# Kernel optimization log

Measured on AMD Instinct MI355X. Metric: run time of the kernel, lower is better.

The kernel has to match this reference:

```python
import jax, jax.numpy as jnp
import numpy as np

HIDDEN = 256
HEADS = 4
HEAD_DIM = HIDDEN // HEADS
SCALE = HEAD_DIM ** -0.5
N1, N2 = 6000, 6000


def setup_inputs() -> dict:
    key = jax.random.key(0)
    ks = jax.random.split(key, 12)
    s = 1.0 / np.sqrt(HIDDEN)
    return {
        "kg1_emb": jax.random.normal(ks[0], (N1, HIDDEN), jnp.float32),
        "kg2_emb": jax.random.normal(ks[1], (N2, HIDDEN), jnp.float32),
        "alignment_matrix": jax.random.bernoulli(ks[2], 0.01, (N1, N2)).astype(jnp.float32),
        "Wq": jax.random.normal(ks[3], (HIDDEN, HIDDEN), jnp.float32) * s,
        "bq": jnp.zeros((HIDDEN,), jnp.float32),
        "Wk": jax.random.normal(ks[4], (HIDDEN, HIDDEN), jnp.float32) * s,
        "bk": jnp.zeros((HIDDEN,), jnp.float32),
        "Wv": jax.random.normal(ks[5], (HIDDEN, HIDDEN), jnp.float32) * s,
        "bv": jnp.zeros((HIDDEN,), jnp.float32),
        "Wo": jax.random.normal(ks[6], (HIDDEN, HIDDEN), jnp.float32) * s,
        "bo": jnp.zeros((HIDDEN,), jnp.float32),
    }


def _cross_attend(q_emb, kv_emb, align, Wq, bq, Wk, bk, Wv, bv):
    # q_emb: [Nq, H*D], kv_emb: [Nk, H*D], align: [Nq, Nk]
    Nq, Nk = q_emb.shape[0], kv_emb.shape[0]
    Q = (q_emb @ Wq.T + bq).reshape(Nq, HEADS, HEAD_DIM)
    K = (kv_emb @ Wk.T + bk).reshape(Nk, HEADS, HEAD_DIM)
    V = (kv_emb @ Wv.T + bv).reshape(Nk, HEADS, HEAD_DIM)
    # einsum('nih,mjh->nmij').mean(-1) == Q against head-mean of K (same math)
    Kbar = K.mean(axis=1)  # [Nk, D]
    scores = jnp.einsum('nid,md->nmi', Q, Kbar) * SCALE  # [Nq, Nk, HEADS]
    scores = scores * align[:, :, None]                  # multiplicative mask
    w = jax.nn.softmax(scores, axis=1)                   # over kv entities
    out = jnp.einsum('nmh,mhd->nhd', w, V)               # [Nq, HEADS, D]
    return out.reshape(Nq, HIDDEN)


def reference(kg1_emb, kg2_emb, alignment_matrix, Wq, bq, Wk, bk, Wv, bv, Wo, bo):
    kg1_from_kg2 = _cross_attend(kg1_emb, kg2_emb, alignment_matrix,
                                 Wq, bq, Wk, bk, Wv, bv)
    kg1_enhanced = kg1_emb + (kg1_from_kg2 @ Wo.T + bo)
    kg2_from_kg1 = _cross_attend(kg2_emb, kg1_emb, alignment_matrix.T,
                                 Wq, bq, Wk, bk, Wv, bv)
    kg2_enhanced = kg2_emb + (kg2_from_kg1 @ Wo.T + bo)
    return (kg1_enhanced, kg2_enhanced)
```

## Files before the change

### kernel.cpp

```cpp
#include <hip/hip_runtime.h>
#include <hip/hip_bf16.h>
#include <stdint.h>

typedef __bf16 bf16_t;
typedef __bf16 bf16x8 __attribute__((ext_vector_type(8)));
typedef __bf16 bf16x4 __attribute__((ext_vector_type(4)));
typedef float f32x4 __attribute__((ext_vector_type(4)));

#define NROW 6000
#define HID 256
#define NHEAD 4
#define HD 64
#define ATT_SCALE 0.125f
#define MTOT 12000
#define CAP 128
#define NCHUNK 4500000

__global__ __launch_bounds__(256)
void detect_kernel(const unsigned short* __restrict__ a, int* __restrict__ flag)
{
    int k = blockIdx.x * 256 + threadIdx.x;
    int found = (k < 102400 && a[2 * k] != 0) ? 1 : 0;
    if (__ballot(found)) {
        if ((threadIdx.x & 63) == 0) atomicOr(flag, 1);
    }
}

__global__ __launch_bounds__(256)
void canon_all_kernel(const void* __restrict__ e1, const void* __restrict__ e2,
                      const void* __restrict__ wq, const void* __restrict__ wk,
                      const void* __restrict__ wv, const void* __restrict__ wo,
                      const void* __restrict__ bq, const void* __restrict__ bk,
                      const void* __restrict__ bv, const void* __restrict__ bo,
                      bf16_t* __restrict__ cE, bf16_t* __restrict__ cWB,
                      const int* __restrict__ flag)
{
    __shared__ int fb;
    if (threadIdx.x == 0) fb = *flag;
    __syncthreads();
    int i = blockIdx.x * 256 + threadIdx.x;
    const int NE = NROW * HID;
    const int NW = 4 * HID * HID;
    auto conv = [&](const void* s, int k) -> bf16_t {
        return fb ? ((const bf16_t*)s)[k] : (bf16_t)(((const float*)s)[k]);
    };
    if (i < 2 * NE) {
        cE[i] = (i < NE) ? conv(e1, i) : conv(e2, i - NE);
        return;
    }
    i -= 2 * NE;
    if (i < NW) {
        int seg = i >> 16; int k = i & 65535;
        const void* s = (seg == 0) ? wq : (seg == 1) ? wk : (seg == 2) ? wv : wo;
        cWB[i] = conv(s, k);
        return;
    }
    i -= NW;
    if (i < 4 * HID) {
        int seg = i >> 8; int k = i & 255;
        const void* s = (seg == 0) ? bq : (seg == 1) ? bk : (seg == 2) ? bv : bo;
        cWB[NW + i] = conv(s, k);
    }
}

__global__ __launch_bounds__(256)
void proj_qkv_kernel(const bf16_t* __restrict__ e12,
                     const bf16_t* __restrict__ wq, const bf16_t* __restrict__ wk,
                     const bf16_t* __restrict__ wv,
                     const bf16_t* __restrict__ bq, const bf16_t* __restrict__ bk,
                     const bf16_t* __restrict__ bv,
                     float* __restrict__ Q, bf16_t* __restrict__ Kf, bf16_t* __restrict__ V)
{
    int m0   = blockIdx.x * 64;
    int n0   = blockIdx.y * 64;
    int wave = threadIdx.x >> 6;
    int lane = threadIdx.x & 63;
    int r16  = lane & 15;
    int quad = lane >> 4;

    int sel = n0 >> 8;
    int jb  = n0 & 255;
    const bf16_t* W; const bf16_t* bias;
    if (sel == 0)      { W = wq; bias = bq; }
    else if (sel == 1) { W = wk; bias = bk; }
    else               { W = wv; bias = bv; }

    int arow = m0 + wave * 16 + r16;
    int rr   = arow < MTOT ? arow : MTOT - 1;
    const bf16_t* asrc = e12 + (size_t)rr * HID;

    f32x4 acc0 = {0,0,0,0}, acc1 = {0,0,0,0}, acc2 = {0,0,0,0}, acc3 = {0,0,0,0};
#pragma unroll
    for (int kk = 0; kk < HID; kk += 32) {
        bf16x8 a = *(const bf16x8*)(asrc + kk + quad * 8);
        const bf16_t* b0 = W + (size_t)(jb + r16) * HID + kk + quad * 8;
        bf16x8 f0 = *(const bf16x8*)(b0);
        bf16x8 f1 = *(const bf16x8*)(b0 + 16 * HID);
        bf16x8 f2 = *(const bf16x8*)(b0 + 32 * HID);
        bf16x8 f3 = *(const bf16x8*)(b0 + 48 * HID);
        acc0 = __builtin_amdgcn_mfma_f32_16x16x32_bf16(a, f0, acc0, 0, 0, 0);
        acc1 = __builtin_amdgcn_mfma_f32_16x16x32_bf16(a, f1, acc1, 0, 0, 0);
        acc2 = __builtin_amdgcn_mfma_f32_16x16x32_bf16(a, f2, acc2, 0, 0, 0);
        acc3 = __builtin_amdgcn_mfma_f32_16x16x32_bf16(a, f3, acc3, 0, 0, 0);
    }
    f32x4 accs[4] = {acc0, acc1, acc2, acc3};
    int rbase = m0 + wave * 16 + quad * 4;
#pragma unroll
    for (int nt = 0; nt < 4; ++nt) {
        int j = jb + nt * 16 + r16;
        float bb = (float)bias[j];
#pragma unroll
        for (int rg = 0; rg < 4; ++rg) {
            int r = rbase + rg;
            if (r < MTOT) {
                float v = accs[nt][rg] + bb;
                if (sel == 0)      Q [(size_t)r * HID + j] = v;
                else if (sel == 1) Kf[(size_t)r * HID + j] = (bf16_t)v;
                else               V [(size_t)r * HID + j] = (bf16_t)v;
            }
        }
    }
}

__global__ __launch_bounds__(256)
void kbar_vsum_kernel(const bf16_t* __restrict__ Kf, const bf16_t* __restrict__ V,
                      bf16_t* __restrict__ Kbar, float* __restrict__ Vsum)
{
    int b = blockIdx.x;
    if (b < 3000) {
        int id = b * 256 + threadIdx.x;
        int m = id >> 6, d = id & 63;
        const bf16_t* kr = Kf + (size_t)m * HID + d;
        Kbar[id] = (bf16_t)(0.25f * ((float)kr[0] + (float)kr[64] +
                                     (float)kr[128] + (float)kr[192]));
    } else {
        int idx = b - 3000;
        int g = idx >> 5 ? 1 : (idx >= 24 ? 1 : 0);
        g = idx / 24;
        int seg = idx - g * 24;
        int j = threadIdx.x;
        const bf16_t* base = V + ((size_t)(g * NROW + seg * 250)) * HID + j;
        float s = 0.f;
        for (int m = 0; m < 250; ++m) s += (float)base[(size_t)m * HID];
        atomicAdd(Vsum + g * HID + j, s);
    }
}

__global__ __launch_bounds__(256)
void scan_nz_kernel(const void* __restrict__ av,
                    int* __restrict__ rcur,
                    int* __restrict__ csr,
                    const int* __restrict__ flag)
{
    __shared__ int fb;
    if (threadIdx.x == 0) fb = *flag;
    __syncthreads();
    int lane = threadIdx.x & 63;
    int ch   = blockIdx.x * 256 + threadIdx.x;
    bool oob = (ch >= NCHUNK);
    int che  = oob ? (NCHUNK - 1) : ch;

    unsigned int nzmask = 0;
    if (!oob) {
        if (fb) {
            uint4 u = *(const uint4*)((const unsigned short*)av + (size_t)che * 8);
            unsigned int w[4] = {u.x, u.y, u.z, u.w};
#pragma unroll
            for (int p = 0; p < 4; ++p) {
                if (w[p] & 0xFFFFu)  nzmask |= 1u << (2 * p);
                if (w[p] >> 16)      nzmask |= 1u << (2 * p + 1);
            }
        } else {
            const unsigned int* aw = (const unsigned int*)av + (size_t)che * 8;
            uint4 u0 = *(const uint4*)(aw);
            uint4 u1 = *(const uint4*)(aw + 4);
            unsigned int w[8] = {u0.x, u0.y, u0.z, u0.w, u1.x, u1.y, u1.z, u1.w};
#pragma unroll
            for (int p = 0; p < 8; ++p)
                if (w[p]) nzmask |= 1u << p;
        }
    }
    int n  = che / 750;
    int m0 = (che - n * 750) * 8;
    int c  = __popc(nzmask);

    int p = c;
#pragma unroll
    for (int off = 1; off < 64; off <<= 1) {
        int t = __shfl_up(p, off);
        if (lane >= off) p += t;
    }
    int excl  = p - c;
    int total = __shfl(p, 63);

    int nFirst = __shfl(n, 0);
    int nLast  = __shfl(n, 63);
    unsigned long long mb = __ballot(n == nLast);
    int s0  = __ffsll(mb) - 1;
    int pS0 = __shfl(excl, s0);

    int baseB = 0;
    if (lane == s0) {
        int totalB = total - pS0;
        if (totalB > 0) baseB = atomicAdd(rcur + nLast, totalB);
    }
    baseB = __shfl(baseB, s0);
    int baseA = 0;
    if (s0 > 0) {
        if (lane == 0 && pS0 > 0) baseA = atomicAdd(rcur + nFirst, pS0);
        baseA = __shfl(baseA, 0);
    }

    int myOff = (n == nLast) ? (baseB + excl - pS0) : (baseA + excl);
    if (c) {
        int* dst = csr + (size_t)n * CAP;
        int w = 0;
#pragma unroll
        for (int pb = 0; pb < 8; ++pb) {
            if (nzmask & (1u << pb)) {
                int idx = myOff + (w++);
                if (idx < CAP) dst[idx] = m0 + pb;
            }
        }
    }
}

__global__ __launch_bounds__(256)
void csc_kernel(const int* __restrict__ rcnt, const int* __restrict__ csr,
                int* __restrict__ ccur, int* __restrict__ csc)
{
    int tid = blockIdx.x * 256 + threadIdx.x;
    int n = tid >> 7, j = tid & (CAP - 1);
    if (n >= NROW) return;
    int cnt = rcnt[n]; if (cnt > CAP) cnt = CAP;
    if (j >= cnt) return;
    int m = csr[(size_t)n * CAP + j];
    int slot = atomicAdd(ccur + m, 1);
    if (slot < CAP) csc[(size_t)m * CAP + slot] = n;
}

__global__ __launch_bounds__(256)
void attn_kernel(const float* __restrict__ Q, const bf16_t* __restrict__ Kbar,
                 const bf16_t* __restrict__ V, const float* __restrict__ Vsum,
                 const int* __restrict__ rcnt, const int* __restrict__ ccnt,
                 const int* __restrict__ csr, const int* __restrict__ csc,
                 bf16_t* __restrict__ att)
{
    __shared__ float qs[HID];
    __shared__ int   ml[CAP];
    __shared__ float sc[CAP * 5];
    __shared__ float w0s[NHEAD];
    __shared__ __align__(16) bf16_t kbs[CAP * HD];

    int dir = blockIdx.y;
    int n   = blockIdx.x;
    int t   = threadIdx.x;
    int wave = t >> 6, lane = t & 63;

    size_t qrow = (size_t)(dir ? NROW + n : n);
    const bf16_t* kb_base = Kbar + (dir ? 0 : (size_t)NROW * HD);
    const bf16_t* v_base  = V    + (dir ? 0 : (size_t)NROW * HID);
    const float*  vs      = Vsum + (dir ? 0 : HID);
    const int*    lst     = (dir ? csc : csr) + (size_t)n * CAP;
    int cnt = (dir ? ccnt : rcnt)[n];
    if (cnt > CAP) cnt = CAP;

    qs[t] = Q[qrow * HID + t];
    for (int j = t; j < cnt; j += 256) ml[j] = lst[j];
    __syncthreads();

    for (int j = wave; j < cnt; j += 4) {
        int m = ml[j];
        bf16_t v = kb_base[(size_t)m * HD + lane];
        kbs[j * HD + ((((lane >> 3) + j) & 7) << 3) + (lane & 7)] = v;
    }
    __syncthreads();

    {
        int head = wave;
        const float* qh = qs + head * HD;
        for (int jb2 = 0; jb2 < cnt; jb2 += 64) {
            int j = jb2 + lane;
            if (j < cnt) {
                float dot = 0.f;
#pragma unroll
                for (int c = 0; c < 8; ++c) {
                    bf16x8 k8 = *(const bf16x8*)(kbs + j * HD + (((c + j) & 7) << 3));
#pragma unroll
                    for (int i = 0; i < 8; ++i)
                        dot += qh[c * 8 + i] * (float)k8[i];
                }
                sc[j * 5 + head] = dot * ATT_SCALE;
            }
        }
    }
    __syncthreads();

    {
        int head = wave;
        float M = 0.0f;
        for (int j = lane; j < cnt; j += 64) M = fmaxf(M, sc[j * 5 + head]);
        for (int off = 32; off; off >>= 1) M = fmaxf(M, __shfl_xor(M, off));
        float e0 = __expf(-M);
        float e[2]; int k = 0;
        float S = 0.f;
        for (int j = lane; j < cnt; j += 64, ++k) { e[k] = __expf(sc[j * 5 + head] - M); S += e[k]; }
        for (int off = 32; off; off >>= 1) S += __shfl_xor(S, off);
        float Z = S + (float)(NROW - cnt) * e0;
        float invZ = 1.0f / Z;
        k = 0;
        for (int j = lane; j < cnt; j += 64, ++k) sc[j * 5 + head] = (e[k] - e0) * invZ;
        if (lane == 0) w0s[head] = e0 * invZ;
    }
    __syncthreads();

    int h3 = lane >> 4;
    int dq = lane & 15;
    int colb = h3 * HD + dq * 4;
    float a0 = 0.f, a1 = 0.f, a2 = 0.f, a3 = 0.f;
    {
        int j = wave;
        for (; j + 4 < cnt; j += 8) {
            int   m0 = ml[j];            int   m1 = ml[j + 4];
            float c0 = sc[j * 5 + h3];   float c1 = sc[(j + 4) * 5 + h3];
            bf16x4 r0 = *(const bf16x4*)(v_base + (size_t)m0 * HID + colb);
            bf16x4 r1 = *(const bf16x4*)(v_base + (size_t)m1 * HID + colb);
            a0 += c0 * (float)r0[0] + c1 * (float)r1[0];
            a1 += c0 * (float)r0[1] + c1 * (float)r1[1];
            a2 += c0 * (float)r0[2] + c1 * (float)r1[2];
            a3 += c0 * (float)r0[3] + c1 * (float)r1[3];
        }
        if (j < cnt) {
            int   m0 = ml[j];
            float c0 = sc[j * 5 + h3];
            bf16x4 r0 = *(const bf16x4*)(v_base + (size_t)m0 * HID + colb);
            a0 += c0 * (float)r0[0];
            a1 += c0 * (float)r0[1];
            a2 += c0 * (float)r0[2];
            a3 += c0 * (float)r0[3];
        }
    }
    __syncthreads();
    float* red = (float*)kbs;
    red[wave * 256 + colb + 0] = a0;
    red[wave * 256 + colb + 1] = a1;
    red[wave * 256 + colb + 2] = a2;
    red[wave * 256 + colb + 3] = a3;
    __syncthreads();
    float tot = red[t] + red[256 + t] + red[512 + t] + red[768 + t]
              + w0s[t >> 6] * vs[t];
    att[qrow * HID + t] = (bf16_t)tot;
}

__global__ __launch_bounds__(256)
void proj_out_kernel(const bf16_t* __restrict__ att, const bf16_t* __restrict__ wo,
                     const bf16_t* __restrict__ bo,
                     const void* __restrict__ e1v, const void* __restrict__ e2v,
                     void* __restrict__ outv, const int* __restrict__ flag)
{
    __shared__ int fb;
    if (threadIdx.x == 0) fb = *flag;
    __syncthreads();

    int m0   = blockIdx.x * 64;
    int n0   = blockIdx.y * 64;
    int wave = threadIdx.x >> 6;
    int lane = threadIdx.x & 63;
    int r16  = lane & 15;
    int quad = lane >> 4;

    int arow = m0 + wave * 16 + r16;
    int rr   = arow < MTOT ? arow : MTOT - 1;
    const bf16_t* asrc = att + (size_t)rr * HID;

    f32x4 acc0 = {0,0,0,0}, acc1 = {0,0,0,0}, acc2 = {0,0,0,0}, acc3 = {0,0,0,0};
#pragma unroll
    for (int kk = 0; kk < HID; kk += 32) {
        bf16x8 a = *(const bf16x8*)(asrc + kk + quad * 8);
        const bf16_t* b0 = wo + (size_t)(n0 + r16) * HID + kk + quad * 8;
        bf16x8 f0 = *(const bf16x8*)(b0);
        bf16x8 f1 = *(const bf16x8*)(b0 + 16 * HID);
        bf16x8 f2 = *(const bf16x8*)(b0 + 32 * HID);
        bf16x8 f3 = *(const bf16x8*)(b0 + 48 * HID);
        acc0 = __builtin_amdgcn_mfma_f32_16x16x32_bf16(a, f0, acc0, 0, 0, 0);
        acc1 = __builtin_amdgcn_mfma_f32_16x16x32_bf16(a, f1, acc1, 0, 0, 0);
        acc2 = __builtin_amdgcn_mfma_f32_16x16x32_bf16(a, f2, acc2, 0, 0, 0);
        acc3 = __builtin_amdgcn_mfma_f32_16x16x32_bf16(a, f3, acc3, 0, 0, 0);
    }
    f32x4 accs[4] = {acc0, acc1, acc2, acc3};
    int rbase = m0 + wave * 16 + quad * 4;
#pragma unroll
    for (int nt = 0; nt < 4; ++nt) {
        int j = n0 + nt * 16 + r16;
        float bb = (float)bo[j];
#pragma unroll
        for (int rg = 0; rg < 4; ++rg) {
            int r = rbase + rg;
            if (r < MTOT) {
                const void* eb = (r < NROW) ? e1v : e2v;
                size_t eidx = (size_t)((r < NROW) ? r : r - NROW) * HID + j;
                float ev = fb ? (float)((const bf16_t*)eb)[eidx]
                              : ((const float*)eb)[eidx];
                float v = accs[nt][rg] + bb + ev;
                size_t oidx = (size_t)r * HID + j;
                if (fb) ((bf16_t*)outv)[oidx] = (bf16_t)v;
                else    ((float*)outv)[oidx]  = v;
            }
        }
    }
}

extern "C" void kernel_launch(void* const* d_in, const int* in_sizes, int n_in,
                              void* d_out, int out_size, void* d_ws, size_t ws_size,
                              hipStream_t stream)
{
    const void* e1v = d_in[0];
    const void* e2v = d_in[1];
    const void* alv = d_in[2];
    const void* wqv = d_in[3];
    const void* bqv = d_in[4];
    const void* wkv = d_in[5];
    const void* bkv = d_in[6];
    const void* wvv = d_in[7];
    const void* bvv = d_in[8];
    const void* wov = d_in[9];
    const void* bov = d_in[10];

    size_t off = 0;
    char* base = (char*)d_ws;
    auto alloc = [&](size_t bytes) -> void* {
        void* p = base + off;
        off += (bytes + 255) & ~(size_t)255;
        return p;
    };
    float*  Q    = (float*) alloc((size_t)MTOT * HID * 4);
    bf16_t* Kf   = (bf16_t*)alloc((size_t)MTOT * HID * 2);
    bf16_t* V    = (bf16_t*)alloc((size_t)MTOT * HID * 2);
    bf16_t* Kbar = (bf16_t*)alloc((size_t)MTOT * HD * 2);
    bf16_t* att  = (bf16_t*)alloc((size_t)MTOT * HID * 2);
    bf16_t* cE   = (bf16_t*)alloc((size_t)MTOT * HID * 2);
    bf16_t* cWB  = (bf16_t*)alloc((size_t)(4 * HID * HID + 4 * HID) * 2);
    int*    csr  = (int*)   alloc((size_t)NROW * CAP * 4);
    int*    csc  = (int*)   alloc((size_t)NROW * CAP * 4);
    int*    flag = (int*)   alloc(256);
    int*    rcur = (int*)   alloc(NROW * 4);
    int*    ccur = (int*)   alloc(NROW * 4);
    float*  Vsum = (float*) alloc(2 * HID * 4);

    bf16_t* cWq = cWB;
    bf16_t* cWk = cWB + 1 * HID * HID;
    bf16_t* cWv = cWB + 2 * HID * HID;
    bf16_t* cWo = cWB + 3 * HID * HID;
    bf16_t* cB  = cWB + 4 * HID * HID;

    size_t zero_bytes = (size_t)((char*)Vsum - (char*)flag) + 2 * HID * 4;
    hipMemsetAsync(flag, 0, zero_bytes, stream);

    detect_kernel<<<400, 256, 0, stream>>>((const unsigned short*)alv, flag);

    const int NTOTC = 2 * NROW * HID + 4 * HID * HID + 4 * HID;
    canon_all_kernel<<<(NTOTC + 255) / 256, 256, 0, stream>>>(
        e1v, e2v, wqv, wkv, wvv, wov, bqv, bkv, bvv, bov, cE, cWB, flag);

    proj_qkv_kernel<<<dim3(188, 12), 256, 0, stream>>>(
        cE, cWq, cWk, cWv, cB, cB + HID, cB + 2 * HID, Q, Kf, V);
    kbar_vsum_kernel<<<3048, 256, 0, stream>>>(Kf, V, Kbar, Vsum);

    scan_nz_kernel<<<(NCHUNK + 255) / 256, 256, 0, stream>>>(alv, rcur, csr, flag);
    csc_kernel<<<(NROW * CAP) / 256, 256, 0, stream>>>(rcur, csr, ccur, csc);

    attn_kernel<<<dim3(NROW, 2), 256, 0, stream>>>(
        Q, Kbar, V, Vsum, rcur, ccur, csr, csc, att);

    proj_out_kernel<<<dim3(188, 4), 256, 0, stream>>>(
        att, cWo, cB + 3 * HID, e1v, e2v, d_out, flag);
}
```

Measured before the change: 421.9 us.

## Drop dtype detection and fuse fp32-to-bf16 conversion into QKV projection

Removes the runtime bf16/fp32 detection kernel and the full embedding canonicalisation pass, assuming fp32 inputs. The embeddings are now converted to bf16 inside the QKV projection's load loop, so the conversion no longer needs its own kernel. Q is stored as bf16 instead of fp32 to halve its traffic, and the mask scan gains an early all-zero check. In exchange, inputs in any other dtype are no longer handled, and Q loses some precision.

```diff
diff --git a/kernel.cpp b/kernel.cpp
--- a/kernel.cpp
+++ b/kernel.cpp
@@ -17,59 +17,22 @@
 #define NCHUNK 4500000
 
 __global__ __launch_bounds__(256)
-void detect_kernel(const unsigned short* __restrict__ a, int* __restrict__ flag)
-{
-    int k = blockIdx.x * 256 + threadIdx.x;
-    int found = (k < 102400 && a[2 * k] != 0) ? 1 : 0;
-    if (__ballot(found)) {
-        if ((threadIdx.x & 63) == 0) atomicOr(flag, 1);
-    }
-}
-
-__global__ __launch_bounds__(256)
-void canon_all_kernel(const void* __restrict__ e1, const void* __restrict__ e2,
-                      const void* __restrict__ wq, const void* __restrict__ wk,
-                      const void* __restrict__ wv, const void* __restrict__ wo,
-                      const void* __restrict__ bq, const void* __restrict__ bk,
-                      const void* __restrict__ bv, const void* __restrict__ bo,
-                      bf16_t* __restrict__ cE, bf16_t* __restrict__ cWB,
-                      const int* __restrict__ flag)
-{
-    __shared__ int fb;
-    if (threadIdx.x == 0) fb = *flag;
-    __syncthreads();
+void canon_w_kernel(const float* __restrict__ wq, const float* __restrict__ wk,
+                    const float* __restrict__ wv, const float* __restrict__ wo,
+                    bf16_t* __restrict__ cW)
+{
     int i = blockIdx.x * 256 + threadIdx.x;
-    const int NE = NROW * HID;
-    const int NW = 4 * HID * HID;
-    auto conv = [&](const void* s, int k) -> bf16_t {
-        return fb ? ((const bf16_t*)s)[k] : (bf16_t)(((const float*)s)[k]);
-    };
-    if (i < 2 * NE) {
-        cE[i] = (i < NE) ? conv(e1, i) : conv(e2, i - NE);
-        return;
-    }
-    i -= 2 * NE;
-    if (i < NW) {
-        int seg = i >> 16; int k = i & 65535;
-        const void* s = (seg == 0) ? wq : (seg == 1) ? wk : (seg == 2) ? wv : wo;
-        cWB[i] = conv(s, k);
-        return;
-    }
-    i -= NW;
-    if (i < 4 * HID) {
-        int seg = i >> 8; int k = i & 255;
-        const void* s = (seg == 0) ? bq : (seg == 1) ? bk : (seg == 2) ? bv : bo;
-        cWB[NW + i] = conv(s, k);
-    }
-}
-
-__global__ __launch_bounds__(256)
-void proj_qkv_kernel(const bf16_t* __restrict__ e12,
-                     const bf16_t* __restrict__ wq, const bf16_t* __restrict__ wk,
-                     const bf16_t* __restrict__ wv,
-                     const bf16_t* __restrict__ bq, const bf16_t* __restrict__ bk,
-                     const bf16_t* __restrict__ bv,
-                     float* __restrict__ Q, bf16_t* __restrict__ Kf, bf16_t* __restrict__ V)
+    int seg = i >> 16, k = i & 65535;
+    const float* s = (seg == 0) ? wq : (seg == 1) ? wk : (seg == 2) ? wv : wo;
+    cW[i] = (bf16_t)s[k];
+}
+
+__global__ __launch_bounds__(256)
+void proj_qkv_kernel(const float* __restrict__ e1, const float* __restrict__ e2,
+                     const bf16_t* __restrict__ cW,
+                     const float* __restrict__ bq, const float* __restrict__ bk,
+                     const float* __restrict__ bv,
+                     bf16_t* __restrict__ Q, bf16_t* __restrict__ Kf, bf16_t* __restrict__ V)
 {
     int m0   = blockIdx.x * 64;
     int n0   = blockIdx.y * 64;
@@ -80,19 +43,22 @@
 
     int sel = n0 >> 8;
     int jb  = n0 & 255;
-    const bf16_t* W; const bf16_t* bias;
-    if (sel == 0)      { W = wq; bias = bq; }
-    else if (sel == 1) { W = wk; bias = bk; }
-    else               { W = wv; bias = bv; }
+    const bf16_t* W = cW + (size_t)sel * HID * HID;
+    const float* bias = (sel == 0) ? bq : (sel == 1) ? bk : bv;
 
     int arow = m0 + wave * 16 + r16;
     int rr   = arow < MTOT ? arow : MTOT - 1;
-    const bf16_t* asrc = e12 + (size_t)rr * HID;
+    const float* asrc = (rr < NROW) ? (e1 + (size_t)rr * HID)
+                                    : (e2 + (size_t)(rr - NROW) * HID);
 
     f32x4 acc0 = {0,0,0,0}, acc1 = {0,0,0,0}, acc2 = {0,0,0,0}, acc3 = {0,0,0,0};
 #pragma unroll
     for (int kk = 0; kk < HID; kk += 32) {
-        bf16x8 a = *(const bf16x8*)(asrc + kk + quad * 8);
+        f32x4 af0 = *(const f32x4*)(asrc + kk + quad * 8);
+        f32x4 af1 = *(const f32x4*)(asrc + kk + quad * 8 + 4);
+        bf16x8 a;
+#pragma unroll
+        for (int i = 0; i < 4; ++i) { a[i] = (bf16_t)af0[i]; a[4 + i] = (bf16_t)af1[i]; }
         const bf16_t* b0 = W + (size_t)(jb + r16) * HID + kk + quad * 8;
         bf16x8 f0 = *(const bf16x8*)(b0);
         bf16x8 f1 = *(const bf16x8*)(b0 + 16 * HID);
@@ -104,20 +70,17 @@
         acc3 = __builtin_amdgcn_mfma_f32_16x16x32_bf16(a, f3, acc3, 0, 0, 0);
     }
     f32x4 accs[4] = {acc0, acc1, acc2, acc3};
+    bf16_t* dst = (sel == 0) ? Q : (sel == 1) ? Kf : V;
     int rbase = m0 + wave * 16 + quad * 4;
 #pragma unroll
     for (int nt = 0; nt < 4; ++nt) {
         int j = jb + nt * 16 + r16;
-        float bb = (float)bias[j];
+        float bb = bias[j];
 #pragma unroll
         for (int rg = 0; rg < 4; ++rg) {
             int r = rbase + rg;
-            if (r < MTOT) {
-                float v = accs[nt][rg] + bb;
-                if (sel == 0)      Q [(size_t)r * HID + j] = v;
-                else if (sel == 1) Kf[(size_t)r * HID + j] = (bf16_t)v;
-                else               V [(size_t)r * HID + j] = (bf16_t)v;
-            }
+            if (r < MTOT)
+                dst[(size_t)r * HID + j] = (bf16_t)(accs[nt][rg] + bb);
         }
     }
 }
@@ -135,8 +98,7 @@
                                      (float)kr[128] + (float)kr[192]));
     } else {
         int idx = b - 3000;
-        int g = idx >> 5 ? 1 : (idx >= 24 ? 1 : 0);
-        g = idx / 24;
+        int g = idx / 24;
         int seg = idx - g * 24;
         int j = threadIdx.x;
         const bf16_t* base = V + ((size_t)(g * NROW + seg * 250)) * HID + j;
@@ -147,14 +109,10 @@
 }
 
 __global__ __launch_bounds__(256)
-void scan_nz_kernel(const void* __restrict__ av,
+void scan_nz_kernel(const float* __restrict__ am,
                     int* __restrict__ rcur,
-                    int* __restrict__ csr,
-                    const int* __restrict__ flag)
-{
-    __shared__ int fb;
-    if (threadIdx.x == 0) fb = *flag;
-    __syncthreads();
+                    int* __restrict__ csr)
+{
     int lane = threadIdx.x & 63;
     int ch   = blockIdx.x * 256 + threadIdx.x;
     bool oob = (ch >= NCHUNK);
@@ -162,18 +120,11 @@
 
     unsigned int nzmask = 0;
     if (!oob) {
-        if (fb) {
-            uint4 u = *(const uint4*)((const unsigned short*)av + (size_t)che * 8);
-            unsigned int w[4] = {u.x, u.y, u.z, u.w};
-#pragma unroll
-            for (int p = 0; p < 4; ++p) {
-                if (w[p] & 0xFFFFu)  nzmask |= 1u << (2 * p);
-                if (w[p] >> 16)      nzmask |= 1u << (2 * p + 1);
-            }
-        } else {
-            const unsigned int* aw = (const unsigned int*)av + (size_t)che * 8;
-            uint4 u0 = *(const uint4*)(aw);
-            uint4 u1 = *(const uint4*)(aw + 4);
+        const unsigned int* aw = (const unsigned int*)am + (size_t)che * 8;
+        uint4 u0 = *(const uint4*)(aw);
+        uint4 u1 = *(const uint4*)(aw + 4);
+        unsigned int any = u0.x | u0.y | u0.z | u0.w | u1.x | u1.y | u1.z | u1.w;
+        if (any) {
             unsigned int w[8] = {u0.x, u0.y, u0.z, u0.w, u1.x, u1.y, u1.z, u1.w};
 #pragma unroll
             for (int p = 0; p < 8; ++p)
@@ -240,7 +191,7 @@
 }
 
 __global__ __launch_bounds__(256)
-void attn_kernel(const float* __restrict__ Q, const bf16_t* __restrict__ Kbar,
+void attn_kernel(const bf16_t* __restrict__ Q, const bf16_t* __restrict__ Kbar,
                  const bf16_t* __restrict__ V, const float* __restrict__ Vsum,
                  const int* __restrict__ rcnt, const int* __restrict__ ccnt,
                  const int* __restrict__ csr, const int* __restrict__ csc,
@@ -265,7 +216,7 @@
     int cnt = (dir ? ccnt : rcnt)[n];
     if (cnt > CAP) cnt = CAP;
 
-    qs[t] = Q[qrow * HID + t];
+    qs[t] = (float)Q[qrow * HID + t];
     for (int j = t; j < cnt; j += 256) ml[j] = lst[j];
     __syncthreads();
 
@@ -354,14 +305,10 @@
 
 __global__ __launch_bounds__(256)
 void proj_out_kernel(const bf16_t* __restrict__ att, const bf16_t* __restrict__ wo,
-                     const bf16_t* __restrict__ bo,
-                     const void* __restrict__ e1v, const void* __restrict__ e2v,
-                     void* __restrict__ outv, const int* __restrict__ flag)
-{
-    __shared__ int fb;
-    if (threadIdx.x == 0) fb = *flag;
-    __syncthreads();
-
+                     const float* __restrict__ bo,
+                     const float* __restrict__ e1, const float* __restrict__ e2,
+                     float* __restrict__ out)
+{
     int m0   = blockIdx.x * 64;
     int n0   = blockIdx.y * 64;
     int wave = threadIdx.x >> 6;
@@ -392,19 +339,15 @@
 #pragma unroll
     for (int nt = 0; nt < 4; ++nt) {
         int j = n0 + nt * 16 + r16;
-        float bb = (float)bo[j];
+        float bb = bo[j];
 #pragma unroll
         for (int rg = 0; rg < 4; ++rg) {
             int r = rbase + rg;
             if (r < MTOT) {
-                const void* eb = (r < NROW) ? e1v : e2v;
-                size_t eidx = (size_t)((r < NROW) ? r : r - NROW) * HID + j;
-                float ev = fb ? (float)((const bf16_t*)eb)[eidx]
-                              : ((const float*)eb)[eidx];
-                float v = accs[nt][rg] + bb + ev;
-                size_t oidx = (size_t)r * HID + j;
-                if (fb) ((bf16_t*)outv)[oidx] = (bf16_t)v;
-                else    ((float*)outv)[oidx]  = v;
+                const float* emb = (r < NROW) ? (e1 + (size_t)r * HID)
+                                              : (e2 + (size_t)(r - NROW) * HID);
+                float v = accs[nt][rg] + bb + emb[j];
+                out[(size_t)r * HID + j] = v;
             }
         }
     }
@@ -414,17 +357,18 @@
                               void* d_out, int out_size, void* d_ws, size_t ws_size,
                               hipStream_t stream)
 {
-    const void* e1v = d_in[0];
-    const void* e2v = d_in[1];
-    const void* alv = d_in[2];
-    const void* wqv = d_in[3];
-    const void* bqv = d_in[4];
-    const void* wkv = d_in[5];
-    const void* bkv = d_in[6];
-    const void* wvv = d_in[7];
-    const void* bvv = d_in[8];
-    const void* wov = d_in[9];
-    const void* bov = d_in[10];
+    const float* e1 = (const float*)d_in[0];
+    const float* e2 = (const float*)d_in[1];
+    const float* am = (const float*)d_in[2];
+    const float* wq = (const float*)d_in[3];
+    const float* bq = (const float*)d_in[4];
+    const float* wk = (const float*)d_in[5];
+    const float* bk = (const float*)d_in[6];
+    const float* wv = (const float*)d_in[7];
+    const float* bv = (const float*)d_in[8];
+    const float* wo = (const float*)d_in[9];
+    const float* bo = (const float*)d_in[10];
+    float* out = (float*)d_out;
 
     size_t off = 0;
     char* base = (char*)d_ws;
@@ -433,45 +377,33 @@
         off += (bytes + 255) & ~(size_t)255;
         return p;
     };
-    float*  Q    = (float*) alloc((size_t)MTOT * HID * 4);
+    bf16_t* Q    = (bf16_t*)alloc((size_t)MTOT * HID * 2);
     bf16_t* Kf   = (bf16_t*)alloc((size_t)MTOT * HID * 2);
     bf16_t* V    = (bf16_t*)alloc((size_t)MTOT * HID * 2);
     bf16_t* Kbar = (bf16_t*)alloc((size_t)MTOT * HD * 2);
     bf16_t* att  = (bf16_t*)alloc((size_t)MTOT * HID * 2);
-    bf16_t* cE   = (bf16_t*)alloc((size_t)MTOT * HID * 2);
-    bf16_t* cWB  = (bf16_t*)alloc((size_t)(4 * HID * HID + 4 * HID) * 2);
+    bf16_t* cW   = (bf16_t*)alloc((size_t)4 * HID * HID * 2);
     int*    csr  = (int*)   alloc((size_t)NROW * CAP * 4);
     int*    csc  = (int*)   alloc((size_t)NROW * CAP * 4);
-    int*    flag = (int*)   alloc(256);
     int*    rcur = (int*)   alloc(NROW * 4);
     int*    ccur = (int*)   alloc(NROW * 4);
     float*  Vsum = (float*) alloc(2 * HID * 4);
 
-    bf16_t* cWq = cWB;
-    bf16_t* cWk = cWB + 1 * HID * HID;
-    bf16_t* cWv = cWB + 2 * HID * HID;
-    bf16_t* cWo = cWB + 3 * HID * HID;
-    bf16_t* cB  = cWB + 4 * HID * HID;
-
-    size_t zero_bytes = (size_t)((char*)Vsum - (char*)flag) + 2 * HID * 4;
-    hipMemsetAsync(flag, 0, zero_bytes, stream);
-
-    detect_kernel<<<400, 256, 0, stream>>>((const unsigned short*)alv, flag);
-
-    const int NTOTC = 2 * NROW * HID + 4 * HID * HID + 4 * HID;
-    canon_all_kernel<<<(NTOTC + 255) / 256, 256, 0, stream>>>(
-        e1v, e2v, wqv, wkv, wvv, wov, bqv, bkv, bvv, bov, cE, cWB, flag);
+    size_t zero_bytes = (size_t)((char*)Vsum - (char*)rcur) + 2 * HID * 4;
+    hipMemsetAsync(rcur, 0, zero_bytes, stream);
+
+    canon_w_kernel<<<1024, 256, 0, stream>>>(wq, wk, wv, wo, cW);
 
     proj_qkv_kernel<<<dim3(188, 12), 256, 0, stream>>>(
-        cE, cWq, cWk, cWv, cB, cB + HID, cB + 2 * HID, Q, Kf, V);
+        e1, e2, cW, bq, bk, bv, Q, Kf, V);
+
     kbar_vsum_kernel<<<3048, 256, 0, stream>>>(Kf, V, Kbar, Vsum);
 
-    scan_nz_kernel<<<(NCHUNK + 255) / 256, 256, 0, stream>>>(alv, rcur, csr, flag);
+    scan_nz_kernel<<<(NCHUNK + 255) / 256, 256, 0, stream>>>(am, rcur, csr);
     csc_kernel<<<(NROW * CAP) / 256, 256, 0, stream>>>(rcur, csr, ccur, csc);
 
     attn_kernel<<<dim3(NROW, 2), 256, 0, stream>>>(
         Q, Kbar, V, Vsum, rcur, ccur, csr, csc, att);
 
-    proj_out_kernel<<<dim3(188, 4), 256, 0, stream>>>(
-        att, cWo, cB + 3 * HID, e1v, e2v, d_out, flag);
-}
+    proj_out_kernel<<<dim3(188, 4), 256, 0, stream>>>(att, cW + 3 * HID * HID, bo, e1, e2, out);
+}
```

Measured after the change: 421.1 us. About the same (-0.2%).
